# Kernel optimization log

Measured on AMD Instinct MI355X. Metric: run time of the kernel, lower is better.

Reference implementation:

```python
import jax, jax.numpy as jnp
import numpy as np

# Circuit hyperparameters (match init_kwargs)
N_QUBITS = 10
N_LAYERS = 5          # hardware_efficient_ansatz layers (data re-uploading)
N_ACTIONS = 2         # CartPole-v1 discrete action space
BETA = 1.0
DIM = 2 ** N_QUBITS

# Bit table: wire 0 is the most-significant bit (PennyLane convention).
_bits = ((np.arange(DIM)[:, None] >> (N_QUBITS - 1 - np.arange(N_QUBITS))) & 1)

# Diagonal of the ring of CZ gates: product over pairs (i, i+1 mod n) of (-1)^{b_i b_j}.
_s = np.ones(DIM)
for _i in range(N_QUBITS):
    _j = (_i + 1) % N_QUBITS
    _s *= 1.0 - 2.0 * (_bits[:, _i] * _bits[:, _j])
CZ_DIAG = jnp.asarray(_s, dtype=jnp.complex64)

# Z^{\otimes n} observable diagonal: (-1)^{popcount(k)}
Z_SIGN = jnp.asarray(1.0 - 2.0 * (_bits.sum(1) % 2), dtype=jnp.float32)


def _rx(t):
    c = jnp.cos(0.5 * t).astype(jnp.complex64)
    s = jnp.sin(0.5 * t).astype(jnp.complex64)
    return jnp.stack([jnp.stack([c, -1j * s], -1), jnp.stack([-1j * s, c], -1)], -2)


def _ry(t):
    c = jnp.cos(0.5 * t).astype(jnp.complex64)
    s = jnp.sin(0.5 * t).astype(jnp.complex64)
    return jnp.stack([jnp.stack([c, -s], -1), jnp.stack([s, c], -1)], -2)


def _rz(t):
    e = jnp.exp(-0.5j * t.astype(jnp.complex64))
    z = jnp.zeros_like(e)
    return jnp.stack([jnp.stack([e, z], -1), jnp.stack([z, jnp.conj(e)], -1)], -2)


def _apply_1q(state, U, q):
    """Apply a single-qubit gate on wire q. state: [B, 2^n]; U: [2,2] or [B,2,2]."""
    B = state.shape[0]
    s = state.reshape(B, 2 ** q, 2, -1)
    if U.ndim == 2:
        s = jnp.einsum('ij,bljr->blir', U, s)
    else:
        s = jnp.einsum('bij,bljr->blir', U, s)
    return s.reshape(B, DIM)


def _variational_layer(state, t):
    """Per-qubit Rx,Ry,Rz rotations (t: [n_qubits,3]) followed by a CZ ring."""
    for q in range(N_QUBITS):
        U = _rz(t[q, 2]) @ _ry(t[q, 1]) @ _rx(t[q, 0])  # RX applied first
        state = _apply_1q(state, U, q)
    return state * CZ_DIAG


def setup_inputs() -> dict:
    key = jax.random.key(0)
    k1, k2 = jax.random.split(key)
    x = jax.random.normal(k1, (2048, N_QUBITS), jnp.float32)
    # _theta = rand(total_theta) * pi ; total_theta = (L+1)*n*3
    theta = jax.random.uniform(k2, ((N_LAYERS + 1) * N_QUBITS * 3,), jnp.float32) * np.pi
    # _lambda = ones(total_inputs) ; total_inputs = L*n
    lam = jnp.ones((N_LAYERS * N_QUBITS,), jnp.float32)
    # Alternating(n_actions): weight row initialized to alternating signs
    w = jnp.asarray([[(-1.0) ** i for i in range(N_ACTIONS)]], jnp.float32)
    return {"x": x, "theta": theta, "lam": lam, "w": w}


def reference(x, theta, lam, w):
    B = x.shape[0]
    th = theta.reshape(N_LAYERS + 1, N_QUBITS, 3)
    lm = lam.reshape(N_LAYERS, N_QUBITS)  # scaled_inputs = x_tiled * lambda
    state = jnp.zeros((B, DIM), jnp.complex64).at[:, 0].set(1.0)
    for l in range(N_LAYERS):
        state = _variational_layer(state, th[l])
        ang = x * lm[l]                      # [B, n] encoding angles for this layer
        for q in range(N_QUBITS):
            state = _apply_1q(state, _rx(ang[:, q]), q)
    state = _variational_layer(state, th[N_LAYERS])
    # <Z x Z x ... x Z>
    exp_z = jnp.sum((state.real ** 2 + state.imag ** 2) * Z_SIGN, axis=1)  # [B]
    logits = exp_z[:, None] * w * BETA       # [B,1] @ [1,n_actions], scaled by beta
    return jax.nn.softmax(logits, axis=1)
```

## Files before the change

### kernel.cpp

```cpp
#include <hip/hip_runtime.h>

#define NQ 10
#define NL 5

typedef float v2f __attribute__((ext_vector_type(2)));

__device__ __forceinline__ v2f sp(float s) { v2f r = { s, s }; return r; }

template <int M>
__device__ __forceinline__ float lane_xor(float v, int lane) {
    unsigned u = __float_as_uint(v);
    if constexpr (M == 1) {
        return __uint_as_float((unsigned)__builtin_amdgcn_update_dpp(0, (int)u, 0xB1, 0xF, 0xF, true));
    } else if constexpr (M == 2) {
        return __uint_as_float((unsigned)__builtin_amdgcn_update_dpp(0, (int)u, 0x4E, 0xF, 0xF, true));
    } else if constexpr (M == 4) {
        return __uint_as_float((unsigned)__builtin_amdgcn_ds_swizzle((int)u, 0x101F));
    } else if constexpr (M == 8) {
        return __uint_as_float((unsigned)__builtin_amdgcn_update_dpp(0, (int)u, 0x128, 0xF, 0xF, true));
    } else if constexpr (M == 16) {
#if __has_builtin(__builtin_amdgcn_permlane16_swap)
        auto r = __builtin_amdgcn_permlane16_swap(u, u, false, false);
        return __uint_as_float((lane & 16) ? r[0] : r[1]);
#else
        return __uint_as_float((unsigned)__builtin_amdgcn_ds_swizzle((int)u, 0x401F));
#endif
    } else {
#if __has_builtin(__builtin_amdgcn_permlane32_swap)
        auto r = __builtin_amdgcn_permlane32_swap(u, u, false, false);
        return __uint_as_float((lane & 32) ? r[0] : r[1]);
#else
        return __shfl_xor(v, 32, 64);
#endif
    }
}

__device__ __forceinline__ void make_u(float tx, float ty, float tz,
                                       float& u00r, float& u00i, float& u01r, float& u01i,
                                       float& u10r, float& u10i, float& u11r, float& u11i) {
    float cx, sx, cy, sy, cz, sz;
    __sincosf(0.5f * tx, &sx, &cx);
    __sincosf(0.5f * ty, &sy, &cy);
    __sincosf(0.5f * tz, &sz, &cz);
    u00r =  cz * cy * cx + sz * sy * sx;
    u00i =  cz * sy * sx - sz * cy * cx;
    u01r = -cz * sy * cx - sz * cy * sx;
    u01i =  sz * sy * cx - cz * cy * sx;
    u10r = -u01r;  u10i =  u01i;
    u11r =  u00r;  u11i = -u00i;
}

__global__ void pqc_setup(const float* __restrict__ theta, float* __restrict__ gm) {
    int g = threadIdx.x;
    if (g >= (NL + 1) * NQ) return;
    const float* th = theta + g * 3;
    float u00r, u00i, u01r, u01i, u10r, u10i, u11r, u11i;
    make_u(th[0], th[1], th[2], u00r, u00i, u01r, u01i, u10r, u10i, u11r, u11i);
    float* o = gm + g * 16;
    o[0] = u00r;  o[1] = u00i;  o[2] = u01r;  o[3] = u01i;
    o[4] = u10r;  o[5] = u10i;  o[6] = u11r;  o[7] = u11i;
    o[8]  = u01i; o[9]  = -u01r; o[10] = u00i; o[11] = -u00r;
    o[12] = u11i; o[13] = -u11r; o[14] = u10i; o[15] = -u10r;
}

template <int P>
__device__ __forceinline__ void apply_p(v2f fr[8], v2f fi[8],
                                        float w00r, float w00i, float w01r, float w01i,
                                        float w10r, float w10i, float w11r, float w11i,
                                        int lane) {
    if constexpr (P == 0) {
        v2f c0r = { w00r, w11r }, c0i = { w00i, w11i };
        v2f c1r = { w01r, w10r }, c1i = { w01i, w10i };
#pragma unroll
        for (int j = 0; j < 8; ++j) {
            v2f ar = fr[j], ai = fi[j];
            v2f srp = ar.yx, sip = ai.yx;
            fr[j] = c0r * ar - c0i * ai + c1r * srp - c1i * sip;
            fi[j] = c0r * ai + c0i * ar + c1r * sip + c1i * srp;
        }
    } else if constexpr (P < 4) {
        constexpr int LJ = 1 << (P - 1);
        v2f a00r = sp(w00r), a00i = sp(w00i), a01r = sp(w01r), a01i = sp(w01i);
        v2f a10r = sp(w10r), a10i = sp(w10i), a11r = sp(w11r), a11i = sp(w11i);
#pragma unroll
        for (int base = 0; base < 8; ++base) {
            if (base & LJ) continue;
            v2f a0r = fr[base], a0i = fi[base];
            v2f a1r = fr[base | LJ], a1i = fi[base | LJ];
            fr[base]      = a00r * a0r - a00i * a0i + a01r * a1r - a01i * a1i;
            fi[base]      = a00r * a0i + a00i * a0r + a01r * a1i + a01i * a1r;
            fr[base | LJ] = a10r * a0r - a10i * a0i + a11r * a1r - a11i * a1i;
            fi[base | LJ] = a10r * a0i + a10i * a0r + a11r * a1i + a11i * a1r;
        }
    } else {
        constexpr int M = 1 << (P - 4);
        const int bit = (lane >> (P - 4)) & 1;
        v2f pr = sp(bit ? w11r : w00r), pi = sp(bit ? w11i : w00i);
        v2f qr = sp(bit ? w10r : w01r), qi = sp(bit ? w10i : w01i);
#pragma unroll
        for (int j = 0; j < 8; ++j) {
            v2f ofr, ofi;
            ofr.x = lane_xor<M>(fr[j].x, lane);
            ofr.y = lane_xor<M>(fr[j].y, lane);
            ofi.x = lane_xor<M>(fi[j].x, lane);
            ofi.y = lane_xor<M>(fi[j].y, lane);
            v2f nr = pr * fr[j] - pi * fi[j] + qr * ofr - qi * ofi;
            v2f ni = pr * fi[j] + pi * fr[j] + qr * ofi + qi * ofr;
            fr[j] = nr;
            fi[j] = ni;
        }
    }
}

__device__ __forceinline__ void apply_q(v2f fr[8], v2f fi[8],
                                        float w00r, float w00i, float w01r, float w01i,
                                        float w10r, float w10i, float w11r, float w11i,
                                        int q, int lane) {
    switch (q) {
        case 0: apply_p<9>(fr, fi, w00r, w00i, w01r, w01i, w10r, w10i, w11r, w11i, lane); break;
        case 1: apply_p<8>(fr, fi, w00r, w00i, w01r, w01i, w10r, w10i, w11r, w11i, lane); break;
        case 2: apply_p<7>(fr, fi, w00r, w00i, w01r, w01i, w10r, w10i, w11r, w11i, lane); break;
        case 3: apply_p<6>(fr, fi, w00r, w00i, w01r, w01i, w10r, w10i, w11r, w11i, lane); break;
        case 4: apply_p<5>(fr, fi, w00r, w00i, w01r, w01i, w10r, w10i, w11r, w11i, lane); break;
        case 5: apply_p<4>(fr, fi, w00r, w00i, w01r, w01i, w10r, w10i, w11r, w11i, lane); break;
        case 6: apply_p<3>(fr, fi, w00r, w00i, w01r, w01i, w10r, w10i, w11r, w11i, lane); break;
        case 7: apply_p<2>(fr, fi, w00r, w00i, w01r, w01i, w10r, w10i, w11r, w11i, lane); break;
        case 8: apply_p<1>(fr, fi, w00r, w00i, w01r, w01i, w10r, w10i, w11r, w11i, lane); break;
        case 9: apply_p<0>(fr, fi, w00r, w00i, w01r, w01i, w10r, w10i, w11r, w11i, lane); break;
    }
}

__global__ void __launch_bounds__(256) pqc_kernel(const float* __restrict__ x,
                                                  const float* __restrict__ lam,
                                                  const float* __restrict__ w,
                                                  const float* __restrict__ gm,
                                                  float* __restrict__ out, int B) {
    const int lane = threadIdx.x & 63;
    const int b = blockIdx.x * (blockDim.x >> 6) + (threadIdx.x >> 6);
    if (b >= B) return;
    const int bu = __builtin_amdgcn_readfirstlane(b);

    v2f fr[8], fi[8];
#pragma unroll
    for (int j = 0; j < 8; ++j) { fr[j] = sp(0.f); fi[j] = sp(0.f); }
    if (lane == 0) fr[0].x = 1.f;

    v2f sv[8];
    unsigned zmask = 0;
#pragma unroll
    for (int j = 0; j < 8; ++j) {
#pragma unroll
        for (int h = 0; h < 2; ++h) {
            int k = (lane << 4) | (2 * j + h);
            int par = (__popc(k & (k >> 1)) + ((k & (k >> 9)) & 1)) & 1;
            float s = __uint_as_float(0x3f800000u | ((unsigned)par << 31));
            if (h == 0) sv[j].x = s; else sv[j].y = s;
            zmask |= (unsigned)(__popc(k) & 1) << (2 * j + h);
        }
    }

    float xr[NQ];
#pragma unroll
    for (int q = 0; q < NQ; ++q) xr[q] = x[bu * NQ + q];

#pragma unroll
    for (int q = 0; q < NQ; ++q) {
        const float* g = gm + q * 16;
        apply_q(fr, fi, g[0], g[1], g[2], g[3], g[4], g[5], g[6], g[7], q, lane);
    }
#pragma unroll
    for (int j = 0; j < 8; ++j) { fr[j] *= sv[j]; fi[j] *= sv[j]; }

#pragma unroll
    for (int l = 1; l <= NL; ++l) {
        const float* lm = lam + (l - 1) * NQ;
#pragma unroll
        for (int q = 0; q < NQ; ++q) {
            const float* g = gm + (l * NQ + q) * 16;
            float t = xr[q] * lm[q];
            float c, s;
            __sincosf(0.5f * t, &s, &c);
            float w00r = c * g[0] + s * g[8],  w00i = c * g[1] + s * g[9];
            float w01r = c * g[2] + s * g[10], w01i = c * g[3] + s * g[11];
            float w10r = c * g[4] + s * g[12], w10i = c * g[5] + s * g[13];
            float w11r = c * g[6] + s * g[14], w11i = c * g[7] + s * g[15];
            apply_q(fr, fi, w00r, w00i, w01r, w01i, w10r, w10i, w11r, w11i, q, lane);
        }
#pragma unroll
        for (int j = 0; j < 8; ++j) { fr[j] *= sv[j]; fi[j] *= sv[j]; }
    }

    v2f acc = sp(0.f);
#pragma unroll
    for (int j = 0; j < 8; ++j) {
        v2f zs;
        zs.x = __uint_as_float(0x3f800000u | (((zmask >> (2 * j)) & 1u) << 31));
        zs.y = __uint_as_float(0x3f800000u | (((zmask >> (2 * j + 1)) & 1u) << 31));
        acc += zs * (fr[j] * fr[j] + fi[j] * fi[j]);
    }
    float ez = acc.x + acc.y;
#pragma unroll
    for (int off = 32; off > 0; off >>= 1) ez += __shfl_xor(ez, off, 64);

    if (lane == 0) {
        float l0 = ez * w[0], l1 = ez * w[1];
        float m = fmaxf(l0, l1);
        float e0 = __expf(l0 - m), e1 = __expf(l1 - m);
        float inv = 1.f / (e0 + e1);
        out[2 * b + 0] = e0 * inv;
        out[2 * b + 1] = e1 * inv;
    }
}

extern "C" void kernel_launch(void* const* d_in, const int* in_sizes, int n_in,
                              void* d_out, int out_size, void* d_ws, size_t ws_size,
                              hipStream_t stream) {
    const float* x     = (const float*)d_in[0];
    const float* theta = (const float*)d_in[1];
    const float* lam   = (const float*)d_in[2];
    const float* w     = (const float*)d_in[3];
    float* out = (float*)d_out;
    float* gm  = (float*)d_ws;

    const int B = in_sizes[0] / NQ;
    hipLaunchKernelGGL(pqc_setup, dim3(1), dim3(64), 0, stream, theta, gm);

    const int wavesPerBlock = 256 / 64;
    const int blocks = (B + wavesPerBlock - 1) / wavesPerBlock;
    hipLaunchKernelGGL(pqc_kernel, dim3(blocks), dim3(256), 0, stream,
                       x, lam, w, gm, out, B);
}
```

Before: 91.85 us.

## Split each sample's statevector across two waves with LDS exchange for qubit 0

Each batch sample now runs on a 128-thread block of two wavefronts instead of one wavefront, so each thread holds 8 amplitudes instead of 16. Gates on qubits 1-9 stay in-register or use cross-lane DPP/swizzle. The qubit-0 gate, whose partner amplitudes now sit in the other wave, swaps halves through double-buffered shared memory with a block barrier. The final expectation value is reduced with DPP lane shuffles and then combined across the two waves in shared memory. The aim is twice as many waves, for better latency hiding and lower register pressure, at the cost of six block barriers and LDS traffic per sample.

```diff
diff --git a/kernel.cpp b/kernel.cpp
--- a/kernel.cpp
+++ b/kernel.cpp
@@ -64,7 +64,7 @@
 }
 
 template <int P>
-__device__ __forceinline__ void apply_p(v2f fr[8], v2f fi[8],
+__device__ __forceinline__ void apply_p(v2f fr[4], v2f fi[4],
                                         float w00r, float w00i, float w01r, float w01i,
                                         float w10r, float w10i, float w11r, float w11i,
                                         int lane) {
@@ -72,18 +72,18 @@
         v2f c0r = { w00r, w11r }, c0i = { w00i, w11i };
         v2f c1r = { w01r, w10r }, c1i = { w01i, w10i };
 #pragma unroll
-        for (int j = 0; j < 8; ++j) {
+        for (int j = 0; j < 4; ++j) {
             v2f ar = fr[j], ai = fi[j];
             v2f srp = ar.yx, sip = ai.yx;
             fr[j] = c0r * ar - c0i * ai + c1r * srp - c1i * sip;
             fi[j] = c0r * ai + c0i * ar + c1r * sip + c1i * srp;
         }
-    } else if constexpr (P < 4) {
+    } else if constexpr (P < 3) {
         constexpr int LJ = 1 << (P - 1);
         v2f a00r = sp(w00r), a00i = sp(w00i), a01r = sp(w01r), a01i = sp(w01i);
         v2f a10r = sp(w10r), a10i = sp(w10i), a11r = sp(w11r), a11i = sp(w11i);
 #pragma unroll
-        for (int base = 0; base < 8; ++base) {
+        for (int base = 0; base < 4; ++base) {
             if (base & LJ) continue;
             v2f a0r = fr[base], a0i = fi[base];
             v2f a1r = fr[base | LJ], a1i = fi[base | LJ];
@@ -93,12 +93,12 @@
             fi[base | LJ] = a10r * a0i + a10i * a0r + a11r * a1i + a11i * a1r;
         }
     } else {
-        constexpr int M = 1 << (P - 4);
-        const int bit = (lane >> (P - 4)) & 1;
+        constexpr int M = 1 << (P - 3);
+        const int bit = (lane >> (P - 3)) & 1;
         v2f pr = sp(bit ? w11r : w00r), pi = sp(bit ? w11i : w00i);
         v2f qr = sp(bit ? w10r : w01r), qi = sp(bit ? w10i : w01i);
 #pragma unroll
-        for (int j = 0; j < 8; ++j) {
+        for (int j = 0; j < 4; ++j) {
             v2f ofr, ofi;
             ofr.x = lane_xor<M>(fr[j].x, lane);
             ofr.y = lane_xor<M>(fr[j].y, lane);
@@ -112,12 +112,36 @@
     }
 }
 
-__device__ __forceinline__ void apply_q(v2f fr[8], v2f fi[8],
+__device__ __forceinline__ void apply_p9(v2f fr[4], v2f fi[4],
+                                         float w00r, float w00i, float w01r, float w01i,
+                                         float w10r, float w10i, float w11r, float w11i,
+                                         int h, int lane, float* buf) {
+    float* mine = buf + h * 128 + lane * 2;
+#pragma unroll
+    for (int j = 0; j < 4; ++j) {
+        *(v2f*)(mine + j * 256)       = fr[j];
+        *(v2f*)(mine + (4 + j) * 256) = fi[j];
+    }
+    __syncthreads();
+    const float* part = buf + (1 - h) * 128 + lane * 2;
+    v2f pr = sp(h ? w11r : w00r), pi = sp(h ? w11i : w00i);
+    v2f qr = sp(h ? w10r : w01r), qi = sp(h ? w10i : w01i);
+#pragma unroll
+    for (int j = 0; j < 4; ++j) {
+        v2f ofr = *(const v2f*)(part + j * 256);
+        v2f ofi = *(const v2f*)(part + (4 + j) * 256);
+        v2f nr = pr * fr[j] - pi * fi[j] + qr * ofr - qi * ofi;
+        v2f ni = pr * fi[j] + pi * fr[j] + qr * ofi + qi * ofr;
+        fr[j] = nr;
+        fi[j] = ni;
+    }
+}
+
+__device__ __forceinline__ void apply_q(v2f fr[4], v2f fi[4],
                                         float w00r, float w00i, float w01r, float w01i,
                                         float w10r, float w10i, float w11r, float w11i,
                                         int q, int lane) {
     switch (q) {
-        case 0: apply_p<9>(fr, fi, w00r, w00i, w01r, w01i, w10r, w10i, w11r, w11i, lane); break;
         case 1: apply_p<8>(fr, fi, w00r, w00i, w01r, w01i, w10r, w10i, w11r, w11i, lane); break;
         case 2: apply_p<7>(fr, fi, w00r, w00i, w01r, w01i, w10r, w10i, w11r, w11i, lane); break;
         case 3: apply_p<6>(fr, fi, w00r, w00i, w01r, w01i, w10r, w10i, w11r, w11i, lane); break;
@@ -130,46 +154,50 @@
     }
 }
 
-__global__ void __launch_bounds__(256) pqc_kernel(const float* __restrict__ x,
+__global__ void __launch_bounds__(128) pqc_kernel(const float* __restrict__ x,
                                                   const float* __restrict__ lam,
                                                   const float* __restrict__ w,
                                                   const float* __restrict__ gm,
                                                   float* __restrict__ out, int B) {
+    __shared__ float lds[2][2048];
     const int lane = threadIdx.x & 63;
-    const int b = blockIdx.x * (blockDim.x >> 6) + (threadIdx.x >> 6);
-    if (b >= B) return;
-    const int bu = __builtin_amdgcn_readfirstlane(b);
-
-    v2f fr[8], fi[8];
-#pragma unroll
-    for (int j = 0; j < 8; ++j) { fr[j] = sp(0.f); fi[j] = sp(0.f); }
-    if (lane == 0) fr[0].x = 1.f;
-
-    v2f sv[8];
+    const int h = threadIdx.x >> 6;
+    const int b = blockIdx.x;
+
+    v2f fr[4], fi[4];
+#pragma unroll
+    for (int j = 0; j < 4; ++j) { fr[j] = sp(0.f); fi[j] = sp(0.f); }
+    if (h == 0 && lane == 0) fr[0].x = 1.f;
+
+    v2f sv[4];
     unsigned zmask = 0;
 #pragma unroll
-    for (int j = 0; j < 8; ++j) {
-#pragma unroll
-        for (int h = 0; h < 2; ++h) {
-            int k = (lane << 4) | (2 * j + h);
+    for (int j = 0; j < 4; ++j) {
+#pragma unroll
+        for (int e = 0; e < 2; ++e) {
+            int k = (h << 9) | (lane << 3) | (2 * j + e);
             int par = (__popc(k & (k >> 1)) + ((k & (k >> 9)) & 1)) & 1;
             float s = __uint_as_float(0x3f800000u | ((unsigned)par << 31));
-            if (h == 0) sv[j].x = s; else sv[j].y = s;
-            zmask |= (unsigned)(__popc(k) & 1) << (2 * j + h);
+            if (e == 0) sv[j].x = s; else sv[j].y = s;
+            zmask |= (unsigned)(__popc(k) & 1) << (2 * j + e);
         }
     }
 
     float xr[NQ];
 #pragma unroll
-    for (int q = 0; q < NQ; ++q) xr[q] = x[bu * NQ + q];
-
-#pragma unroll
-    for (int q = 0; q < NQ; ++q) {
-        const float* g = gm + q * 16;
-        apply_q(fr, fi, g[0], g[1], g[2], g[3], g[4], g[5], g[6], g[7], q, lane);
-    }
-#pragma unroll
-    for (int j = 0; j < 8; ++j) { fr[j] *= sv[j]; fi[j] *= sv[j]; }
+    for (int q = 0; q < NQ; ++q) xr[q] = x[b * NQ + q];
+
+    {
+        const float* g = gm;
+        apply_p9(fr, fi, g[0], g[1], g[2], g[3], g[4], g[5], g[6], g[7], h, lane, lds[0]);
+#pragma unroll
+        for (int q = 1; q < NQ; ++q) {
+            const float* gq = gm + q * 16;
+            apply_q(fr, fi, gq[0], gq[1], gq[2], gq[3], gq[4], gq[5], gq[6], gq[7], q, lane);
+        }
+#pragma unroll
+        for (int j = 0; j < 4; ++j) { fr[j] *= sv[j]; fi[j] *= sv[j]; }
+    }
 
 #pragma unroll
     for (int l = 1; l <= NL; ++l) {
@@ -184,26 +212,36 @@
             float w01r = c * g[2] + s * g[10], w01i = c * g[3] + s * g[11];
             float w10r = c * g[4] + s * g[12], w10i = c * g[5] + s * g[13];
             float w11r = c * g[6] + s * g[14], w11i = c * g[7] + s * g[15];
-            apply_q(fr, fi, w00r, w00i, w01r, w01i, w10r, w10i, w11r, w11i, q, lane);
-        }
-#pragma unroll
-        for (int j = 0; j < 8; ++j) { fr[j] *= sv[j]; fi[j] *= sv[j]; }
+            if (q == 0)
+                apply_p9(fr, fi, w00r, w00i, w01r, w01i, w10r, w10i, w11r, w11i, h, lane, lds[l & 1]);
+            else
+                apply_q(fr, fi, w00r, w00i, w01r, w01i, w10r, w10i, w11r, w11i, q, lane);
+        }
+#pragma unroll
+        for (int j = 0; j < 4; ++j) { fr[j] *= sv[j]; fi[j] *= sv[j]; }
     }
 
     v2f acc = sp(0.f);
 #pragma unroll
-    for (int j = 0; j < 8; ++j) {
+    for (int j = 0; j < 4; ++j) {
         v2f zs;
         zs.x = __uint_as_float(0x3f800000u | (((zmask >> (2 * j)) & 1u) << 31));
         zs.y = __uint_as_float(0x3f800000u | (((zmask >> (2 * j + 1)) & 1u) << 31));
         acc += zs * (fr[j] * fr[j] + fi[j] * fi[j]);
     }
     float ez = acc.x + acc.y;
-#pragma unroll
-    for (int off = 32; off > 0; off >>= 1) ez += __shfl_xor(ez, off, 64);
-
-    if (lane == 0) {
-        float l0 = ez * w[0], l1 = ez * w[1];
+    ez += lane_xor<1>(ez, lane);
+    ez += lane_xor<2>(ez, lane);
+    ez += lane_xor<4>(ez, lane);
+    ez += lane_xor<8>(ez, lane);
+    ez += lane_xor<16>(ez, lane);
+    ez += lane_xor<32>(ez, lane);
+
+    if (lane == 0) lds[0][h] = ez;
+    __syncthreads();
+    if (h == 0 && lane == 0) {
+        float e = lds[0][0] + lds[0][1];
+        float l0 = e * w[0], l1 = e * w[1];
         float m = fmaxf(l0, l1);
         float e0 = __expf(l0 - m), e1 = __expf(l1 - m);
         float inv = 1.f / (e0 + e1);
@@ -224,9 +262,6 @@
 
     const int B = in_sizes[0] / NQ;
     hipLaunchKernelGGL(pqc_setup, dim3(1), dim3(64), 0, stream, theta, gm);
-
-    const int wavesPerBlock = 256 / 64;
-    const int blocks = (B + wavesPerBlock - 1) / wavesPerBlock;
-    hipLaunchKernelGGL(pqc_kernel, dim3(blocks), dim3(256), 0, stream,
+    hipLaunchKernelGGL(pqc_kernel, dim3(B), dim3(128), 0, stream,
                        x, lam, w, gm, out, B);
 }
```

Result: slower. 100.7 us (+9.6%).

## Use one-wave blocks, batch per-layer gate building, and DPP reduction

Applied to the files above, without the earlier changes.

The kernel now launches one 64-thread block per batch element with launch bounds (64,2), in place of four waves per 256-thread block. For each layer it computes all sincos values and all ten gate matrices up front, then applies the gates in a fixed sequence, so the loads and transcendentals can be scheduled ahead of the dependent state updates. The final reduction uses DPP and swizzle lane exchanges in place of __shfl_xor. Holding the precomputed gate arrays raises register pressure, and the (64,2) launch bounds may change how many waves fit per SIMD.

```diff
diff --git a/kernel.cpp b/kernel.cpp
--- a/kernel.cpp
+++ b/kernel.cpp
@@ -64,10 +64,9 @@
 }
 
 template <int P>
-__device__ __forceinline__ void apply_p(v2f fr[8], v2f fi[8],
-                                        float w00r, float w00i, float w01r, float w01i,
-                                        float w10r, float w10i, float w11r, float w11i,
-                                        int lane) {
+__device__ __forceinline__ void apply_p(v2f fr[8], v2f fi[8], const float wv[8], int lane) {
+    const float w00r = wv[0], w00i = wv[1], w01r = wv[2], w01i = wv[3];
+    const float w10r = wv[4], w10i = wv[5], w11r = wv[6], w11i = wv[7];
     if constexpr (P == 0) {
         v2f c0r = { w00r, w11r }, c0i = { w00i, w11i };
         v2f c1r = { w01r, w10r }, c1i = { w01i, w10i };
@@ -112,33 +111,29 @@
     }
 }
 
-__device__ __forceinline__ void apply_q(v2f fr[8], v2f fi[8],
-                                        float w00r, float w00i, float w01r, float w01i,
-                                        float w10r, float w10i, float w11r, float w11i,
-                                        int q, int lane) {
-    switch (q) {
-        case 0: apply_p<9>(fr, fi, w00r, w00i, w01r, w01i, w10r, w10i, w11r, w11i, lane); break;
-        case 1: apply_p<8>(fr, fi, w00r, w00i, w01r, w01i, w10r, w10i, w11r, w11i, lane); break;
-        case 2: apply_p<7>(fr, fi, w00r, w00i, w01r, w01i, w10r, w10i, w11r, w11i, lane); break;
-        case 3: apply_p<6>(fr, fi, w00r, w00i, w01r, w01i, w10r, w10i, w11r, w11i, lane); break;
-        case 4: apply_p<5>(fr, fi, w00r, w00i, w01r, w01i, w10r, w10i, w11r, w11i, lane); break;
-        case 5: apply_p<4>(fr, fi, w00r, w00i, w01r, w01i, w10r, w10i, w11r, w11i, lane); break;
-        case 6: apply_p<3>(fr, fi, w00r, w00i, w01r, w01i, w10r, w10i, w11r, w11i, lane); break;
-        case 7: apply_p<2>(fr, fi, w00r, w00i, w01r, w01i, w10r, w10i, w11r, w11i, lane); break;
-        case 8: apply_p<1>(fr, fi, w00r, w00i, w01r, w01i, w10r, w10i, w11r, w11i, lane); break;
-        case 9: apply_p<0>(fr, fi, w00r, w00i, w01r, w01i, w10r, w10i, w11r, w11i, lane); break;
-    }
-}
-
-__global__ void __launch_bounds__(256) pqc_kernel(const float* __restrict__ x,
-                                                  const float* __restrict__ lam,
-                                                  const float* __restrict__ w,
-                                                  const float* __restrict__ gm,
-                                                  float* __restrict__ out, int B) {
-    const int lane = threadIdx.x & 63;
-    const int b = blockIdx.x * (blockDim.x >> 6) + (threadIdx.x >> 6);
-    if (b >= B) return;
-    const int bu = __builtin_amdgcn_readfirstlane(b);
+__device__ __forceinline__ void apply_layer(v2f fr[8], v2f fi[8], const float W[NQ][8],
+                                            const v2f sv[8], int lane) {
+    apply_p<9>(fr, fi, W[0], lane);
+    apply_p<8>(fr, fi, W[1], lane);
+    apply_p<7>(fr, fi, W[2], lane);
+    apply_p<6>(fr, fi, W[3], lane);
+    apply_p<5>(fr, fi, W[4], lane);
+    apply_p<4>(fr, fi, W[5], lane);
+    apply_p<3>(fr, fi, W[6], lane);
+    apply_p<2>(fr, fi, W[7], lane);
+    apply_p<1>(fr, fi, W[8], lane);
+    apply_p<0>(fr, fi, W[9], lane);
+#pragma unroll
+    for (int j = 0; j < 8; ++j) { fr[j] *= sv[j]; fi[j] *= sv[j]; }
+}
+
+__global__ void __launch_bounds__(64, 2) pqc_kernel(const float* __restrict__ x,
+                                                    const float* __restrict__ lam,
+                                                    const float* __restrict__ w,
+                                                    const float* __restrict__ gm,
+                                                    float* __restrict__ out, int B) {
+    const int lane = threadIdx.x;
+    const int b = blockIdx.x;
 
     v2f fr[8], fi[8];
 #pragma unroll
@@ -161,33 +156,32 @@
 
     float xr[NQ];
 #pragma unroll
-    for (int q = 0; q < NQ; ++q) xr[q] = x[bu * NQ + q];
-
-#pragma unroll
-    for (int q = 0; q < NQ; ++q) {
-        const float* g = gm + q * 16;
-        apply_q(fr, fi, g[0], g[1], g[2], g[3], g[4], g[5], g[6], g[7], q, lane);
-    }
-#pragma unroll
-    for (int j = 0; j < 8; ++j) { fr[j] *= sv[j]; fi[j] *= sv[j]; }
+    for (int q = 0; q < NQ; ++q) xr[q] = x[b * NQ + q];
+
+    {
+        float W[NQ][8];
+#pragma unroll
+        for (int q = 0; q < NQ; ++q)
+#pragma unroll
+            for (int t = 0; t < 8; ++t) W[q][t] = gm[q * 16 + t];
+        apply_layer(fr, fi, W, sv, lane);
+    }
 
 #pragma unroll
     for (int l = 1; l <= NL; ++l) {
         const float* lm = lam + (l - 1) * NQ;
+        float cc[NQ], ss[NQ];
+#pragma unroll
+        for (int q = 0; q < NQ; ++q)
+            __sincosf(0.5f * xr[q] * lm[q], &ss[q], &cc[q]);
+        float W[NQ][8];
 #pragma unroll
         for (int q = 0; q < NQ; ++q) {
             const float* g = gm + (l * NQ + q) * 16;
-            float t = xr[q] * lm[q];
-            float c, s;
-            __sincosf(0.5f * t, &s, &c);
-            float w00r = c * g[0] + s * g[8],  w00i = c * g[1] + s * g[9];
-            float w01r = c * g[2] + s * g[10], w01i = c * g[3] + s * g[11];
-            float w10r = c * g[4] + s * g[12], w10i = c * g[5] + s * g[13];
-            float w11r = c * g[6] + s * g[14], w11i = c * g[7] + s * g[15];
-            apply_q(fr, fi, w00r, w00i, w01r, w01i, w10r, w10i, w11r, w11i, q, lane);
-        }
-#pragma unroll
-        for (int j = 0; j < 8; ++j) { fr[j] *= sv[j]; fi[j] *= sv[j]; }
+#pragma unroll
+            for (int t = 0; t < 8; ++t) W[q][t] = cc[q] * g[t] + ss[q] * g[8 + t];
+        }
+        apply_layer(fr, fi, W, sv, lane);
     }
 
     v2f acc = sp(0.f);
@@ -199,8 +193,12 @@
         acc += zs * (fr[j] * fr[j] + fi[j] * fi[j]);
     }
     float ez = acc.x + acc.y;
-#pragma unroll
-    for (int off = 32; off > 0; off >>= 1) ez += __shfl_xor(ez, off, 64);
+    ez += lane_xor<1>(ez, lane);
+    ez += lane_xor<2>(ez, lane);
+    ez += lane_xor<4>(ez, lane);
+    ez += lane_xor<8>(ez, lane);
+    ez += lane_xor<16>(ez, lane);
+    ez += lane_xor<32>(ez, lane);
 
     if (lane == 0) {
         float l0 = ez * w[0], l1 = ez * w[1];
@@ -224,9 +222,6 @@
 
     const int B = in_sizes[0] / NQ;
     hipLaunchKernelGGL(pqc_setup, dim3(1), dim3(64), 0, stream, theta, gm);
-
-    const int wavesPerBlock = 256 / 64;
-    const int blocks = (B + wavesPerBlock - 1) / wavesPerBlock;
-    hipLaunchKernelGGL(pqc_kernel, dim3(blocks), dim3(256), 0, stream,
+    hipLaunchKernelGGL(pqc_kernel, dim3(B), dim3(64), 0, stream,
                        x, lam, w, gm, out, B);
 }
```

New measurement: 90.26 us. About the same (-1.7%).
